# Optimization experiments

Measured on AMD Instinct MI355X. Metric: run time of the kernel, lower is better.

The kernel has to match this reference:

```python
import jax, jax.numpy as jnp
import numpy as np

WH, WW, NUM_HEADS = 7, 7, 16
DIM = 512
B_WINDOWS = 4096   # batch * num_windows
NW = 64            # num_windows per image (mask groups)
N = WH * WW        # 49 tokens per window


def _relative_position_index():
    # Mirrors the torch buffer construction exactly (torch.meshgrid default is 'ij').
    coords = np.stack(np.meshgrid(np.arange(WH), np.arange(WW), indexing='ij'))  # [2,WH,WW]
    cf = coords.reshape(2, -1)                              # [2, N]
    rel = cf[:, :, None] - cf[:, None, :]                   # [2, N, N]
    rel = rel.transpose(1, 2, 0).copy()                     # [N, N, 2]
    rel[:, :, 0] += WH - 1
    rel[:, :, 1] += WW - 1
    rel[:, :, 0] *= 2 * WW - 1
    return jnp.asarray(rel.sum(-1), dtype=jnp.int32)        # [N, N]

REL_IDX = _relative_position_index()


def setup_inputs() -> dict:
    key = jax.random.key(0)
    ks = jax.random.split(key, 7)
    return {
        'x':          jax.random.normal(ks[0], (B_WINDOWS, N, DIM), jnp.float32),
        'mask':       jax.random.normal(ks[1], (NW, N, N), jnp.float32),
        'Wqkv':       jax.random.normal(ks[2], (3 * DIM, DIM), jnp.float32) * (DIM ** -0.5),
        'bqkv':       jax.random.normal(ks[3], (3 * DIM,), jnp.float32) * 0.02,
        'bias_table': jax.random.normal(ks[4], ((2 * WH - 1) * (2 * WW - 1), NUM_HEADS), jnp.float32) * 0.02,
        'Wproj':      jax.random.normal(ks[5], (DIM, DIM), jnp.float32) * (DIM ** -0.5),
        'bproj':      jax.random.normal(ks[6], (DIM,), jnp.float32) * 0.02,
    }


def reference(x, mask, Wqkv, bqkv, bias_table, Wproj, bproj):
    B, n, C = x.shape                      # [B_, 49, 512]
    hd = C // NUM_HEADS
    scale = hd ** -0.5
    qkv = (x @ Wqkv.T + bqkv).reshape(B, n, 3, NUM_HEADS, hd)
    qkv = qkv.transpose(2, 0, 3, 1, 4)     # [3, B, H, N, hd]
    q, k, v = qkv[0] * scale, qkv[1], qkv[2]
    attn = jnp.einsum('bhnd,bhmd->bhnm', q, k)          # [B, H, N, N]
    # gathered relative position bias: [1, H, N, N]
    bias = bias_table[REL_IDX].transpose(2, 0, 1)[None]
    attn = attn + bias
    nW = mask.shape[0]
    attn = attn.reshape(B // nW, nW, NUM_HEADS, n, n) + mask[None, :, None]
    attn = jax.nn.softmax(attn.reshape(B, NUM_HEADS, n, n), axis=-1)
    out = jnp.einsum('bhnm,bhmd->bhnd', attn, v)        # [B, H, N, hd]
    out = out.transpose(0, 2, 1, 3).reshape(B, n, C)
    return out @ Wproj.T + bproj
```

## Files before the change

kernel.cpp:

```cpp
#include <hip/hip_runtime.h>
#include <stdint.h>

#define NHEADS 16
#define DIM 512
#define BWIN 4096
#define NTOK 49
#define M_TOTAL (BWIN * NTOK)
#define QSCALE 0.17677669529663687f

typedef __attribute__((ext_vector_type(4)))  float f32x4;
typedef __attribute__((ext_vector_type(16))) float f32x16;
typedef __attribute__((ext_vector_type(8)))  short s16x8;
typedef __attribute__((ext_vector_type(4)))  short s16x4;

__device__ __forceinline__ f32x4 mfma16(s16x8 a, s16x8 b, f32x4 c) {
    return __builtin_amdgcn_mfma_f32_16x16x32_bf16(a, b, c, 0, 0, 0);
}
__device__ __forceinline__ f32x16 mfma32(s16x8 a, s16x8 b, f32x16 c) {
    return __builtin_amdgcn_mfma_f32_32x32x16_bf16(a, b, c, 0, 0, 0);
}

__device__ __forceinline__ short f2bf(float f) {
    unsigned u = __builtin_bit_cast(unsigned, f);
    u += 0x7FFFu + ((u >> 16) & 1u);
    return (short)(u >> 16);
}

__device__ __forceinline__ unsigned cvtpk(float a, float b) {
    unsigned r;
    asm("v_cvt_pk_bf16_f32 %0, %1, %2" : "=v"(r) : "v"(a), "v"(b));
    return r;
}

__device__ __forceinline__ void gload16(const void* g, void* l) {
    __builtin_amdgcn_global_load_lds(
        (const __attribute__((address_space(1))) void*)g,
        (__attribute__((address_space(3))) void*)l, 16, 0, 0);
}


__global__ void k_prep_x(const float* __restrict__ x, short* __restrict__ xb) {
    int i = blockIdx.x * blockDim.x + threadIdx.x;
    int stride = gridDim.x * blockDim.x;
    const int n4 = M_TOTAL * DIM / 4;
    for (; i < n4; i += stride) {
        f32x4 v = ((const f32x4*)x)[i];
        s16x4 o;
        o[0] = f2bf(v[0]); o[1] = f2bf(v[1]); o[2] = f2bf(v[2]); o[3] = f2bf(v[3]);
        ((s16x4*)xb)[i] = o;
    }
}

__global__ void k_prep_w(const float* __restrict__ src, short* __restrict__ dst,
                         int n, int scale_lim) {
    int i = blockIdx.x * blockDim.x + threadIdx.x;
    int stride = gridDim.x * blockDim.x;
    for (; i < n; i += stride) {
        float v = src[i];
        if (i < scale_lim) v *= QSCALE;
        dst[i] = f2bf(v);
    }
}

__global__ void k_prep_bm(const float* __restrict__ btab, const float* __restrict__ mask,
                          float* __restrict__ bmT) {
    int idx = blockIdx.x * blockDim.x + threadIdx.x;
    int stride = gridDim.x * blockDim.x;
    const int n = 64 * NHEADS * 49 * 64;
    for (; idx < n; idx += stride) {
        int i = idx & 63;
        int rest = idx >> 6;
        int j = rest % 49;
        int wh = rest / 49;
        int head = wh & 15;
        int w64 = wh >> 4;
        float v = 0.f;
        if (i < 49) {
            int ridx = (i / 7 - j / 7 + 6) * 13 + (i % 7 - j % 7 + 6);
            v = btab[ridx * 16 + head] + mask[(w64 * 49 + i) * 49 + j];
        }
        bmT[idx] = v;
    }
}

template <int MODE>
__global__ __launch_bounds__(256) void k_gemm(
    const short* __restrict__ A, const short* __restrict__ B,
    const float* __restrict__ bias, void* __restrict__ C,
    int ntiles, int nwg) {
    __shared__ short lA[128 * 64];
    __shared__ short lB[128 * 64];
    const int K = 512;
    const size_t MP = M_TOTAL;

    int bid   = blockIdx.x;
    int chunk = nwg >> 3;
    int wg    = (bid & 7) * chunk + (bid >> 3);
    int mt = wg / ntiles;
    int nt = wg - mt * ntiles;

    int t = threadIdx.x;
    int lane = t & 63, wid = t >> 6;
    int l15 = lane & 15, g = lane >> 4;
    int wm = (wid >> 1) * 64, wn = (wid & 1) * 64;

    int schunk = (t & 7) ^ ((t >> 3) & 7);
    size_t aoff = (size_t)(mt * 128 + (t >> 3)) * K + schunk * 8;
    size_t boff = (size_t)(nt * 128 + (t >> 3)) * K + schunk * 8;
    char* lAb = (char*)lA + wid * 1024;
    char* lBb = (char*)lB + wid * 1024;

    f32x4 acc[4][4] = {};

    for (int k0 = 0; k0 < K; k0 += 64) {
#pragma unroll
        for (int i = 0; i < 4; i++) {
            gload16(A + aoff + k0 + (size_t)i * 32 * K, lAb + i * 4096);
            gload16(B + boff + k0 + (size_t)i * 32 * K, lBb + i * 4096);
        }
        __syncthreads();

        const short* pa = lA + (wm + l15) * 64;
        const short* pb = lB + (wn + l15) * 64;
        const int sw = l15 & 7;
#pragma unroll
        for (int ks = 0; ks < 2; ks++) {
            s16x8 af[4], bf[4];
            const int co = ((ks * 4) ^ 0);
#pragma unroll
            for (int i = 0; i < 4; i++)
                af[i] = *(const s16x8*)(pa + i * 1024 + (((ks * 4 + g) ^ sw) * 8));
#pragma unroll
            for (int i = 0; i < 4; i++)
                bf[i] = *(const s16x8*)(pb + i * 1024 + (((ks * 4 + g) ^ sw) * 8));
#pragma unroll
            for (int i = 0; i < 4; i++)
#pragma unroll
                for (int j = 0; j < 4; j++)
                    acc[i][j] = mfma16(af[i], bf[j], acc[i][j]);
            (void)co;
        }
        __syncthreads();
    }

    int m_base = mt * 128 + wm + (g << 2);
#pragma unroll
    for (int nj = 0; nj < 4; nj++) {
        int nb = nt * 128 + wn + nj * 16;
        float bv = bias[nb + l15];
        if (MODE == 0 && nb < 512) bv *= QSCALE;
#pragma unroll
        for (int mi = 0; mi < 4; mi++) {
#pragma unroll
            for (int r = 0; r < 4; r++) {
                int m = m_base + mi * 16 + r;
                float v = acc[mi][nj][r] + bv;
                if (MODE == 0) {
                    int plane = ((nb >> 9) << 4) | ((nb >> 5) & 15);
                    size_t dst = ((size_t)plane * MP + m) * 32 + (nb & 31) + l15;
                    ((short*)C)[dst] = f2bf(v);
                } else {
                    ((float*)C)[(size_t)m * 512 + nb + l15] = v;
                }
            }
        }
    }
}

__global__ __launch_bounds__(256, 4) void k_attn(
    const short* __restrict__ qkv, const float* __restrict__ bmT,
    short* __restrict__ ao) {
    int wid = threadIdx.x >> 6, lane = threadIdx.x & 63;
    int p = blockIdx.x * 4 + wid;
    int w = p >> 4, head = p & 15;
    int l31 = lane & 31, h = lane >> 5;
    const size_t MP = M_TOTAL;

    const short* qb = qkv + ((size_t)head * MP + w * 49) * 32;
    const short* kb = qb + (size_t)16 * MP * 32;
    const short* vb = qb + (size_t)32 * MP * 32;

    s16x8 qf[2][2], kf[2][2];
#pragma unroll
    for (int t = 0; t < 2; t++) {
        int row = t * 32 + l31;
#pragma unroll
        for (int s = 0; s < 2; s++) {
            qf[t][s] = *(const s16x8*)(qb + row * 32 + 16 * s + 8 * h);
            kf[t][s] = *(const s16x8*)(kb + row * 32 + 16 * s + 8 * h);
        }
    }

    union U8 { short s[8]; s16x8 v; };
    U8 vf[4];
#pragma unroll
    for (int jc = 0; jc < 4; jc++)
#pragma unroll
        for (int e = 0; e < 8; e++)
            vf[jc].s[e] = vb[(16 * jc + 8 * h + e) * 32 + l31];

    f32x16 st[2][2] = {};
#pragma unroll
    for (int s = 0; s < 2; s++)
#pragma unroll
        for (int jt = 0; jt < 2; jt++)
#pragma unroll
            for (int it = 0; it < 2; it++)
                st[jt][it] = mfma32(kf[jt][s], qf[it][s], st[jt][it]);

    const float* bs = bmT + ((size_t)((w & 63) * NHEADS + head)) * 3136 + l31;
#pragma unroll
    for (int jt = 0; jt < 2; jt++)
#pragma unroll
        for (int it = 0; it < 2; it++)
#pragma unroll
            for (int r = 0; r < 16; r++) {
                int j = 32 * jt + (r & 3) + 8 * (r >> 2) + 4 * h;
                if (j < 49) st[jt][it][r] += bs[j * 64 + 32 * it];
                else        st[jt][it][r] = -1e30f;
            }

    float inv[2];
#pragma unroll
    for (int it = 0; it < 2; it++) {
        float mx = -1e30f;
#pragma unroll
        for (int jt = 0; jt < 2; jt++)
#pragma unroll
            for (int r = 0; r < 16; r++) mx = fmaxf(mx, st[jt][it][r]);
        mx = fmaxf(mx, __shfl_xor(mx, 32));
        float sum = 0.f;
#pragma unroll
        for (int jt = 0; jt < 2; jt++)
#pragma unroll
            for (int r = 0; r < 16; r++) {
                float e = __expf(st[jt][it][r] - mx);
                st[jt][it][r] = e;
                sum += e;
            }
        sum += __shfl_xor(sum, 32);
        inv[it] = 1.0f / sum;
    }

    f32x16 oacc[2] = {};
#pragma unroll
    for (int jc = 0; jc < 4; jc++) {
        const int jt = jc >> 1, rb = 8 * (jc & 1);
#pragma unroll
        for (int it = 0; it < 2; it++) {
            float iv = inv[it];
            unsigned pk0  = cvtpk(st[jt][it][rb + 0] * iv, st[jt][it][rb + 1] * iv);
            unsigned pk0b = cvtpk(st[jt][it][rb + 2] * iv, st[jt][it][rb + 3] * iv);
            unsigned pk1  = cvtpk(st[jt][it][rb + 4] * iv, st[jt][it][rb + 5] * iv);
            unsigned pk1b = cvtpk(st[jt][it][rb + 6] * iv, st[jt][it][rb + 7] * iv);
            unsigned o0  = __shfl_xor(pk0, 32);
            unsigned o0b = __shfl_xor(pk0b, 32);
            unsigned o1  = __shfl_xor(pk1, 32);
            unsigned o1b = __shfl_xor(pk1b, 32);
            union { unsigned d[4]; s16x8 v; } pa;
            pa.d[0] = h ? o1  : pk0;
            pa.d[1] = h ? o1b : pk0b;
            pa.d[2] = h ? pk1 : o0;
            pa.d[3] = h ? pk1b : o0b;
            oacc[it] = mfma32(pa.v, vf[jc].v, oacc[it]);
        }
    }

    short* ob = ao + (size_t)w * 49 * 512 + head * 32 + l31;
#pragma unroll
    for (int it = 0; it < 2; it++)
#pragma unroll
        for (int r = 0; r < 16; r++) {
            int i = 32 * it + 4 * h + (r & 3) + 8 * (r >> 2);
            if (i < 49) ob[(size_t)i * 512] = f2bf(oacc[it][r]);
        }
}


extern "C" void kernel_launch(void* const* d_in, const int* in_sizes, int n_in,
                              void* d_out, int out_size, void* d_ws, size_t ws_size,
                              hipStream_t stream) {
    const float* x     = (const float*)d_in[0];
    const float* mask  = (const float*)d_in[1];
    const float* Wqkv  = (const float*)d_in[2];
    const float* bqkv  = (const float*)d_in[3];
    const float* btab  = (const float*)d_in[4];
    const float* Wproj = (const float*)d_in[5];
    const float* bproj = (const float*)d_in[6];
    float* out = (float*)d_out;

    char* ws = (char*)d_ws;
    size_t off = 0;
    short* xb     = (short*)(ws + off); off += (size_t)M_TOTAL * 512 * 2;
    short* qkvb   = (short*)(ws + off); off += (size_t)48 * M_TOTAL * 32 * 2 + 65536;
    short* Wqkvb  = (short*)(ws + off); off += (size_t)1536 * 512 * 2;
    short* Wprojb = (short*)(ws + off); off += (size_t)512 * 512 * 2;
    float* bmT    = (float*)(ws + off); off += (size_t)64 * NHEADS * 49 * 64 * 4;
    short* ao = xb;

    k_prep_x<<<2048, 256, 0, stream>>>(x, xb);
    k_prep_w<<<1536, 256, 0, stream>>>(Wqkv, Wqkvb, 1536 * 512, 512 * 512);
    k_prep_w<<<512, 256, 0, stream>>>(Wproj, Wprojb, 512 * 512, 0);
    k_prep_bm<<<2048, 256, 0, stream>>>(btab, mask, bmT);

    k_gemm<0><<<18816, 256, 0, stream>>>(xb, Wqkvb, bqkv, qkvb, 12, 18816);
    k_attn<<<16384, 256, 0, stream>>>(qkvb, bmT, ao);
    k_gemm<1><<<6272, 256, 0, stream>>>(ao, Wprojb, bproj, out, 4, 6272);
}
```

Measured before the change: 1.304 ms.

## Enlarge GEMM tiles to 256x256 with double-buffered LDS and staged epilogue

The GEMM kernel moves from 128x128 tiles with 256 threads to 256x256 tiles with 512 threads. Global-to-LDS loads are double-buffered with explicit vmcnt waits, so the next K-slice prefetch overlaps MFMA work. The QKV epilogue now stages bf16 results in LDS and writes 16-byte vectorized rows into the per-head plane layout. The larger tile improves operand reuse, but it raises register pressure (32 accumulators per thread) and LDS use to 128KB, which limits occupancy.

```diff
diff --git a/kernel.cpp b/kernel.cpp
--- a/kernel.cpp
+++ b/kernel.cpp
@@ -84,12 +84,12 @@
 }
 
 template <int MODE>
-__global__ __launch_bounds__(256) void k_gemm(
+__global__ __launch_bounds__(512, 2) void k_gemm(
     const short* __restrict__ A, const short* __restrict__ B,
     const float* __restrict__ bias, void* __restrict__ C,
     int ntiles, int nwg) {
-    __shared__ short lA[128 * 64];
-    __shared__ short lB[128 * 64];
+    __shared__ short lA[2][256 * 64];
+    __shared__ short lB[2][256 * 64];
     const int K = 512;
     const size_t MP = M_TOTAL;
 
@@ -101,68 +101,102 @@
 
     int t = threadIdx.x;
     int lane = t & 63, wid = t >> 6;
-    int l15 = lane & 15, g = lane >> 4;
-    int wm = (wid >> 1) * 64, wn = (wid & 1) * 64;
-
-    int schunk = (t & 7) ^ ((t >> 3) & 7);
-    size_t aoff = (size_t)(mt * 128 + (t >> 3)) * K + schunk * 8;
-    size_t boff = (size_t)(nt * 128 + (t >> 3)) * K + schunk * 8;
-    char* lAb = (char*)lA + wid * 1024;
-    char* lBb = (char*)lB + wid * 1024;
-
-    f32x4 acc[4][4] = {};
-
-    for (int k0 = 0; k0 < K; k0 += 64) {
-#pragma unroll
-        for (int i = 0; i < 4; i++) {
-            gload16(A + aoff + k0 + (size_t)i * 32 * K, lAb + i * 4096);
-            gload16(B + boff + k0 + (size_t)i * 32 * K, lBb + i * 4096);
-        }
-        __syncthreads();
-
-        const short* pa = lA + (wm + l15) * 64;
-        const short* pb = lB + (wn + l15) * 64;
+    int l15 = lane & 15, g = (lane >> 4) & 3;
+    int wr = wid >> 2, wc = wid & 3;
+
+    int srow = t >> 3;
+    int schunk = (t & 7) ^ (srow & 7);
+    const short* aSrc = A + (size_t)(mt * 256 + srow) * K + schunk * 8;
+    const short* bSrc = B + (size_t)(nt * 256 + srow) * K + schunk * 8;
+    const int dstOff = t * 8;
+
+    f32x4 acc[8][4] = {};
+
+#define STAGE(buf, k0)                                                        \
+    _Pragma("unroll")                                                         \
+    for (int i = 0; i < 4; i++) {                                             \
+        gload16(aSrc + (size_t)i * 64 * K + (k0), &lA[buf][i * 4096 + dstOff]); \
+        gload16(bSrc + (size_t)i * 64 * K + (k0), &lB[buf][i * 4096 + dstOff]); \
+    }
+
+    STAGE(0, 0)
+    for (int kt = 0; kt < 8; ++kt) {
+        if (kt < 7) {
+            STAGE((kt + 1) & 1, (kt + 1) * 64)
+            asm volatile("s_waitcnt vmcnt(8)" ::: "memory");
+        } else {
+            asm volatile("s_waitcnt vmcnt(0)" ::: "memory");
+        }
+        __builtin_amdgcn_s_barrier();
+
+        const short* pa = &lA[kt & 1][(wr * 128 + l15) * 64];
+        const short* pb = &lB[kt & 1][(wc * 64 + l15) * 64];
         const int sw = l15 & 7;
 #pragma unroll
         for (int ks = 0; ks < 2; ks++) {
-            s16x8 af[4], bf[4];
-            const int co = ((ks * 4) ^ 0);
-#pragma unroll
-            for (int i = 0; i < 4; i++)
-                af[i] = *(const s16x8*)(pa + i * 1024 + (((ks * 4 + g) ^ sw) * 8));
-#pragma unroll
-            for (int i = 0; i < 4; i++)
-                bf[i] = *(const s16x8*)(pb + i * 1024 + (((ks * 4 + g) ^ sw) * 8));
-#pragma unroll
-            for (int i = 0; i < 4; i++)
-#pragma unroll
-                for (int j = 0; j < 4; j++)
-                    acc[i][j] = mfma16(af[i], bf[j], acc[i][j]);
-            (void)co;
-        }
-        __syncthreads();
-    }
-
-    int m_base = mt * 128 + wm + (g << 2);
-#pragma unroll
-    for (int nj = 0; nj < 4; nj++) {
-        int nb = nt * 128 + wn + nj * 16;
-        float bv = bias[nb + l15];
-        if (MODE == 0 && nb < 512) bv *= QSCALE;
-#pragma unroll
-        for (int mi = 0; mi < 4; mi++) {
-#pragma unroll
-            for (int r = 0; r < 4; r++) {
-                int m = m_base + mi * 16 + r;
-                float v = acc[mi][nj][r] + bv;
-                if (MODE == 0) {
-                    int plane = ((nb >> 9) << 4) | ((nb >> 5) & 15);
-                    size_t dst = ((size_t)plane * MP + m) * 32 + (nb & 31) + l15;
-                    ((short*)C)[dst] = f2bf(v);
-                } else {
-                    ((float*)C)[(size_t)m * 512 + nb + l15] = v;
+            s16x8 af[8], bf[4];
+#pragma unroll
+            for (int mi = 0; mi < 8; mi++)
+                af[mi] = *(const s16x8*)(pa + mi * 1024 + (((ks * 4 + g) ^ sw) * 8));
+#pragma unroll
+            for (int nj = 0; nj < 4; nj++)
+                bf[nj] = *(const s16x8*)(pb + nj * 1024 + (((ks * 4 + g) ^ sw) * 8));
+#pragma unroll
+            for (int mi = 0; mi < 8; mi++)
+#pragma unroll
+                for (int nj = 0; nj < 4; nj++)
+                    acc[mi][nj] = mfma16(af[mi], bf[nj], acc[mi][nj]);
+        }
+        __builtin_amdgcn_s_barrier();
+    }
+#undef STAGE
+
+    int m0 = mt * 256 + wr * 128;
+    int n0 = nt * 256 + wc * 64;
+
+    if (MODE == 0) {
+        short* region = (wid < 4) ? (&lA[0][0] + wid * 8192)
+                                  : (&lB[0][0] + (wid - 4) * 8192);
+#pragma unroll
+        for (int nj = 0; nj < 4; nj++) {
+            int n = n0 + nj * 16 + l15;
+            float bv = bias[n];
+            if (n < 512) bv *= QSCALE;
+            int w16 = nj * 2 + (l15 >> 3);
+#pragma unroll
+            for (int mi = 0; mi < 8; mi++)
+#pragma unroll
+                for (int r = 0; r < 4; r++) {
+                    int row = mi * 16 + g * 4 + r;
+                    region[row * 64 + ((w16 ^ (row & 7)) * 8) + (l15 & 7)] =
+                        f2bf(acc[mi][nj][r] + bv);
                 }
+        }
+#pragma unroll
+        for (int p = 0; p < 2; p++) {
+            int plane = (n0 >> 5) + p;
+            short* dst = (short*)C + ((size_t)plane * MP + m0) * 32;
+#pragma unroll
+            for (int i = 0; i < 8; i++) {
+                int f = i * 64 + lane;
+                int row = f >> 2, c = f & 3;
+                s16x8 v = *(const s16x8*)(region + row * 64 +
+                                          (((p * 4 + c) ^ (row & 7)) * 8));
+                *(s16x8*)(dst + (size_t)f * 8) = v;
             }
+        }
+    } else {
+#pragma unroll
+        for (int nj = 0; nj < 4; nj++) {
+            int n = n0 + nj * 16 + l15;
+            float bv = bias[n];
+#pragma unroll
+            for (int mi = 0; mi < 8; mi++)
+#pragma unroll
+                for (int r = 0; r < 4; r++) {
+                    int m = m0 + mi * 16 + g * 4 + r;
+                    ((float*)C)[(size_t)m * 512 + n] = acc[mi][nj][r] + bv;
+                }
         }
     }
 }
@@ -303,7 +337,7 @@
     k_prep_w<<<512, 256, 0, stream>>>(Wproj, Wprojb, 512 * 512, 0);
     k_prep_bm<<<2048, 256, 0, stream>>>(btab, mask, bmT);
 
-    k_gemm<0><<<18816, 256, 0, stream>>>(xb, Wqkvb, bqkv, qkvb, 12, 18816);
+    k_gemm<0><<<4704, 512, 0, stream>>>(xb, Wqkvb, bqkv, qkvb, 6, 4704);
     k_attn<<<16384, 256, 0, stream>>>(qkvb, bmT, ao);
-    k_gemm<1><<<6272, 256, 0, stream>>>(ao, Wprojb, bproj, out, 4, 6272);
-}
+    k_gemm<1><<<1568, 512, 0, stream>>>(ao, Wprojb, bproj, out, 2, 1568);
+}
```

New measurement: 1.178 ms. 1.11x faster.
